# Kernel tuning notes

Hardware: AMD Instinct MI355X
Metric: run time of the kernel (lower is better)

Reference implementation:

```python
import jax, jax.numpy as jnp
import numpy as np

EPS = 1e-5
N_HEADS = 8

def layer_norm(x, g, b):
    mu = x.mean(-1, keepdims=True)
    var = ((x - mu) ** 2).mean(-1, keepdims=True)
    return (x - mu) * jax.lax.rsqrt(var + EPS) * g + b

def rotate_half(x):
    d = x.shape[-1] // 2
    return jnp.concatenate([-x[..., d:], x[..., :d]], axis=-1)

def setup_inputs() -> dict:
    key = jax.random.key(0)
    ks = jax.random.split(key, 6)
    b, n, m, h, dh = 4, 512, 8192, N_HEADS, 16
    dim = h * dh
    s = dim ** -0.5
    return {
        "x": jax.random.normal(ks[0], (b, n, dim), jnp.float32),
        "mem_kv": jax.random.normal(ks[1], (b, h, m, 2 * dh), jnp.float32),
        "w_q": jax.random.normal(ks[2], (dim, dim), jnp.float32) * s,
        "w_kv": jax.random.normal(ks[3], (2 * dim, dim), jnp.float32) * s,
        "w_out": jax.random.normal(ks[4], (dim, dim), jnp.float32) * s,
        "b_out": jnp.zeros((dim,), jnp.float32),
        "g1": jnp.ones((dim,), jnp.float32),
        "b1": jnp.zeros((dim,), jnp.float32),
        "g2": jnp.ones((dim,), jnp.float32),
        "b2": jnp.zeros((dim,), jnp.float32),
    }

def reference(x, mem_kv, w_q, w_kv, w_out, b_out, g1, b1, g2, b2):
    b, n, dim = x.shape
    h = N_HEADS
    dh = dim // h
    # pre-norm + projections
    x_ = layer_norm(x, g1, b1)
    q = (x_ @ w_q.T).reshape(b, n, h, dh).transpose(0, 2, 1, 3)          # [b,h,n,dh]
    kv = (x_ @ w_kv.T).reshape(b, n, h, 2 * dh).transpose(0, 2, 1, 3)    # [b,h,n,2dh]
    mem_kv = jnp.concatenate([mem_kv, kv], axis=2)                        # growing cache
    k, v = jnp.split(mem_kv, 2, axis=-1)                                  # [b,h,j,dh] each
    q = q * dh ** -0.5
    # rotary embeddings (SinusoidalEmbeddings over k length, q uses trailing n positions)
    j = k.shape[2]
    inv_freq = 1.0 / (10000.0 ** (jnp.arange(0, dh, 2, dtype=jnp.float32) / dh))
    fr = jnp.arange(j, dtype=jnp.float32)[:, None] * inv_freq[None, :]
    freqs = jnp.concatenate([fr, fr], axis=-1)                            # [j, dh]
    cos, sin = jnp.cos(freqs), jnp.sin(freqs)
    q = q * cos[-n:] + rotate_half(q) * sin[-n:]
    k = k * cos + rotate_half(k) * sin
    # full attention of new chunk over cache (forward_simple, inference)
    sim = jnp.einsum('bhie,bhje->bhij', q, k)
    attn = jax.nn.softmax(sim, axis=-1)
    hv = jnp.einsum('bhij,bhje->bhie', attn, v)
    hv = hv.transpose(0, 2, 1, 3).reshape(b, n, dim) + x                  # residual
    out = layer_norm(hv, g2, b2) @ w_out.T + b_out + hv                   # out proj + residual
    return out, mem_kv
```

## Files before the change

kernel.cpp:

```cpp
#include <hip/hip_runtime.h>

#define B 4
#define N 512
#define M 8192
#define H 8
#define DH 16
#define DIM 128
#define J (M + N)
#define LN10000_DIV8 1.1512925465f
#define LOG2E 1.44269504f

typedef _Float16 f16;
typedef _Float16 half4 __attribute__((ext_vector_type(4)));
typedef _Float16 half8 __attribute__((ext_vector_type(8)));
typedef __fp16 fp16x2 __attribute__((ext_vector_type(2)));
typedef float f32x4 __attribute__((ext_vector_type(4)));

#if __has_builtin(__builtin_amdgcn_exp2f)
#define EXP2(x) __builtin_amdgcn_exp2f(x)
#else
#define EXP2(x) exp2f(x)
#endif

union PK { fp16x2 v; unsigned int u; };

__device__ __forceinline__ half8 pack8(float a, float b, float c, float d,
                                       float e, float f, float g, float h) {
#if __has_builtin(__builtin_amdgcn_cvt_pkrtz)
    union { unsigned int u[4]; half8 h8; } r;
    PK p0, p1, p2, p3;
    p0.v = __builtin_amdgcn_cvt_pkrtz(a, b);
    p1.v = __builtin_amdgcn_cvt_pkrtz(c, d);
    p2.v = __builtin_amdgcn_cvt_pkrtz(e, f);
    p3.v = __builtin_amdgcn_cvt_pkrtz(g, h);
    r.u[0] = p0.u; r.u[1] = p1.u; r.u[2] = p2.u; r.u[3] = p3.u;
    return r.h8;
#else
    half8 r = { (f16)a, (f16)b, (f16)c, (f16)d, (f16)e, (f16)f, (f16)g, (f16)h };
    return r;
#endif
}

#define WS_KROT 0ull
#define WS_VT   8912896ull
#define WS_QROT 17825792ull
#define WS_HV   18350080ull
#define WS_XN   18874368ull

union K16 { f16 h[16]; uint4 u[2]; };
union V4  { f16 h[4];  uint2 u; };

__device__ __forceinline__ half8 cvt8(const float* p) {
    float4 a = *(const float4*)p, b = *(const float4*)(p + 4);
    half8 h = { (f16)a.x, (f16)a.y, (f16)a.z, (f16)a.w,
                (f16)b.x, (f16)b.y, (f16)b.z, (f16)b.w };
    return h;
}

__global__ void prep_kernel(const float4* __restrict__ src,
                            f16* __restrict__ krot, f16* __restrict__ vt,
                            const float* __restrict__ x, const float* __restrict__ g1,
                            const float* __restrict__ b1, f16* __restrict__ xn16)
{
    if (blockIdx.x < 4096) {
        __shared__ float tile[64][33];
        int bh = blockIdx.x >> 7;
        int j0 = (blockIdx.x & 127) * 64;
        int t = threadIdx.x;

        #pragma unroll
        for (int rep = 0; rep < 2; rep++) {
            int idx = t + rep * 256;
            int row = idx >> 3, c4 = idx & 7;
            float4 v = src[((size_t)bh * M + j0 + row) * 8 + c4];
            tile[row][c4 * 4 + 0] = v.x; tile[row][c4 * 4 + 1] = v.y;
            tile[row][c4 * 4 + 2] = v.z; tile[row][c4 * 4 + 3] = v.w;
        }
        __syncthreads();

        if (t < 128) {
            int row = t >> 1, rh = t & 1;
            int j = j0 + row;
            float lo4[4], hi4[4];
            #pragma unroll
            for (int i = 0; i < 4; i++) {
                int r = rh * 4 + i;
                float ang = (float)j * __expf(-(float)r * LN10000_DIV8);
                float sn, cs; __sincosf(ang, &sn, &cs);
                float lo = tile[row][r], hi = tile[row][r + 8];
                lo4[i] = lo * cs - hi * sn;
                hi4[i] = hi * cs + lo * sn;
            }
            int tilei = j >> 5, jj = j & 31;
            int col4 = (jj >> 3) * 4 + (jj & 3), frag = (jj >> 2) & 1;
            f16* base = krot + (size_t)bh * J * 16 + (size_t)tilei * 512 + col4 * 8 + frag * 4;
            V4 wl, wh;
            #pragma unroll
            for (int i = 0; i < 4; i++) { wl.h[i] = (f16)lo4[i]; wh.h[i] = (f16)hi4[i]; }
            *(uint2*)(base + rh * 128)       = wl.u;
            *(uint2*)(base + (2 + rh) * 128) = wh.u;
        }
        {
            int dh = t >> 4, c0 = (t & 15) * 4;
            V4 vv;
            #pragma unroll
            for (int i = 0; i < 4; i++) vv.h[i] = (f16)tile[c0 + i][16 + dh];
            *(uint2*)(vt + (size_t)bh * 16 * J + (size_t)dh * J + j0 + c0) = vv.u;
        }
    } else {
        int wave = threadIdx.x >> 6, lane = threadIdx.x & 63;
        int token = (blockIdx.x - 4096) * 4 + wave;
        float v0 = x[(size_t)token * DIM + lane];
        float v1 = x[(size_t)token * DIM + lane + 64];
        float s = v0 + v1;
        for (int off = 32; off; off >>= 1) s += __shfl_xor(s, off, 64);
        float mu = s * (1.0f / DIM);
        float d0 = v0 - mu, d1 = v1 - mu;
        float vs = d0 * d0 + d1 * d1;
        for (int off = 32; off; off >>= 1) vs += __shfl_xor(vs, off, 64);
        float rs = rsqrtf(vs * (1.0f / DIM) + 1e-5f);
        xn16[(size_t)token * DIM + lane]      = (f16)(d0 * rs * g1[lane]      + b1[lane]);
        xn16[(size_t)token * DIM + lane + 64] = (f16)(d1 * rs * g1[lane + 64] + b1[lane + 64]);
    }
}

__global__ void __launch_bounds__(256) proj_kernel(
    const f16* __restrict__ xn16, const float* __restrict__ wq,
    const float* __restrict__ wkv, float* __restrict__ out_mem,
    f16* __restrict__ krot, f16* __restrict__ vt, f16* __restrict__ qrot)
{
    int id = blockIdx.x * 4 + (threadIdx.x >> 6);
    int lane = threadIdx.x & 63;
    int ttile = id & 127, ctile = id >> 7;
    int token0 = ttile * 16;
    int col = lane & 15, quad = lane >> 4;

    const float* wbase = (ctile < 8) ? (wq + (size_t)(ctile * 16 + col) * DIM)
                                     : (wkv + (size_t)((ctile - 8) * 16 + col) * DIM);
    const f16* abase = xn16 + (size_t)(token0 + col) * DIM + quad * 8;

    f32x4 acc = {0.f, 0.f, 0.f, 0.f};
    #pragma unroll
    for (int kb = 0; kb < 4; kb++) {
        half8 a = *(const half8*)(abase + kb * 32);
        half8 w = cvt8(wbase + kb * 32 + quad * 8);
        acc = __builtin_amdgcn_mfma_f32_16x16x32_f16(a, w, acc, 0, 0, 0);
    }

    int e = col, r8 = e & 7;
    float f = __expf(-(float)r8 * LN10000_DIV8);
    int kt = ctile - 8;
    int head = (ctile < 8) ? ctile : (kt >> 1);
    int isV  = (ctile >= 8) ? (kt & 1) : 0;

    #pragma unroll
    for (int r = 0; r < 4; r++) {
        int tok = token0 + quad * 4 + r;
        int b = tok >> 9, i = tok & (N - 1);
        int bhh = b * H + head;
        float self = acc[r];
        float prt = __shfl_xor(self, 8, 64);

        if (ctile < 8) {
            float ang = (float)(M + i) * f;
            float sn, cs; __sincosf(ang, &sn, &cs);
            float rv = (self * cs + ((e < 8) ? -prt : prt) * sn) * (0.25f * LOG2E);
            qrot[((size_t)bhh * N + i) * 16 + e] = (f16)rv;
        } else if (!isV) {
            out_mem[((size_t)bhh * J + M + i) * 32 + e] = self;
            float ang = (float)(M + i) * f;
            float sn, cs; __sincosf(ang, &sn, &cs);
            float rv = self * cs + ((e < 8) ? -prt : prt) * sn;
            int jpos = M + i;
            int tilei = jpos >> 5, jj = jpos & 31;
            int col4 = (jj >> 3) * 4 + (jj & 3), frag = (jj >> 2) & 1;
            krot[(size_t)bhh * J * 16 + (size_t)tilei * 512 +
                 (e >> 2) * 128 + col4 * 8 + frag * 4 + (e & 3)] = (f16)rv;
        } else {
            out_mem[((size_t)bhh * J + M + i) * 32 + 16 + e] = self;
            vt[(size_t)bhh * 16 * J + (size_t)e * J + M + i] = (f16)self;
        }
    }
}

__global__ void __launch_bounds__(512, 4) attn_kernel(
    const f16* __restrict__ krot, const f16* __restrict__ vt,
    const f16* __restrict__ qrot, f16* __restrict__ hvw,
    const f32x4* __restrict__ csrc, f32x4* __restrict__ cdst)
{
    __shared__ float sacc[8][2][256];
    __shared__ float sl[8][2][16];

    if (blockIdx.x % 5 != 0) {
        int t = threadIdx.x;
        size_t copyid = (size_t)blockIdx.x - blockIdx.x / 5 - 1;
        size_t base = copyid * 1024;
        #pragma unroll
        for (int rep = 0; rep < 2; rep++) {
            size_t flat = base + rep * 512 + t;
            int bh  = (int)(flat >> 16);
            int rem = (int)(flat & 65535);
            f32x4 v = __builtin_nontemporal_load(csrc + flat);
            __builtin_nontemporal_store(v, cdst + (size_t)bh * (J * 8) + rem);
        }
        return;
    }

    int cid = blockIdx.x / 5;
    int bh = cid & 31;
    int q0 = (cid >> 5) * 32;
    int wave = threadIdx.x >> 6, lane = threadIdx.x & 63;
    int col = lane & 15, quad = lane >> 4;

    const f16* vb = vt + (size_t)bh * 16 * J + (size_t)col * J;
    half4 qfa = *(const half4*)(qrot + ((size_t)bh * N + q0 + col) * 16 + quad * 4);
    half4 qfb = *(const half4*)(qrot + ((size_t)bh * N + q0 + 16 + col) * 16 + quad * 4);

    int jstart = wave * (J / 8);
    const f16* kptr = krot + (size_t)bh * J * 16 + (size_t)jstart * 16 + lane * 8;
    const f16* vptr = vb + jstart + quad * 8;

    f32x4 acca = {0.f, 0.f, 0.f, 0.f};
    f32x4 accb = {0.f, 0.f, 0.f, 0.f};
    const f32x4 zero = {0.f, 0.f, 0.f, 0.f};
    float la = 0.f, lb = 0.f;

    #pragma unroll 2
    for (int it = 0; it < 34; ++it) {
        half8 kf8 = *(const half8*)kptr;
        half8 vf  = *(const half8*)vptr;
        kptr += 512; vptr += 32;
        half4 kf0 = __builtin_shufflevector(kf8, kf8, 0, 1, 2, 3);
        half4 kf1 = __builtin_shufflevector(kf8, kf8, 4, 5, 6, 7);
        __builtin_amdgcn_s_setprio(1);
        f32x4 s0a = __builtin_amdgcn_mfma_f32_16x16x16f16(kf0, qfa, zero, 0, 0, 0);
        f32x4 s1a = __builtin_amdgcn_mfma_f32_16x16x16f16(kf1, qfa, zero, 0, 0, 0);
        f32x4 s0b = __builtin_amdgcn_mfma_f32_16x16x16f16(kf0, qfb, zero, 0, 0, 0);
        f32x4 s1b = __builtin_amdgcn_mfma_f32_16x16x16f16(kf1, qfb, zero, 0, 0, 0);
        __builtin_amdgcn_s_setprio(0);

        float a0 = EXP2(s0a[0]), a1 = EXP2(s0a[1]), a2 = EXP2(s0a[2]), a3 = EXP2(s0a[3]);
        float a4 = EXP2(s1a[0]), a5 = EXP2(s1a[1]), a6 = EXP2(s1a[2]), a7 = EXP2(s1a[3]);
        float b0 = EXP2(s0b[0]), b1 = EXP2(s0b[1]), b2 = EXP2(s0b[2]), b3 = EXP2(s0b[3]);
        float b4 = EXP2(s1b[0]), b5 = EXP2(s1b[1]), b6 = EXP2(s1b[2]), b7 = EXP2(s1b[3]);
        la += ((a0 + a1) + (a2 + a3)) + ((a4 + a5) + (a6 + a7));
        lb += ((b0 + b1) + (b2 + b3)) + ((b4 + b5) + (b6 + b7));
        half8 pfa = pack8(a0, a1, a2, a3, a4, a5, a6, a7);
        half8 pfb = pack8(b0, b1, b2, b3, b4, b5, b6, b7);
        __builtin_amdgcn_s_setprio(1);
        acca = __builtin_amdgcn_mfma_f32_16x16x32_f16(pfa, vf, acca, 0, 0, 0);
        accb = __builtin_amdgcn_mfma_f32_16x16x32_f16(pfb, vf, accb, 0, 0, 0);
        __builtin_amdgcn_s_setprio(0);
    }

    la += __shfl_xor(la, 16, 64);
    la += __shfl_xor(la, 32, 64);
    lb += __shfl_xor(lb, 16, 64);
    lb += __shfl_xor(lb, 32, 64);
    if (quad == 0) { sl[wave][0][col] = la; sl[wave][1][col] = lb; }
    #pragma unroll
    for (int r = 0; r < 4; r++) {
        sacc[wave][0][(quad * 4 + r) * 16 + col] = acca[r];
        sacc[wave][1][(quad * 4 + r) * 16 + col] = accb[r];
    }
    __syncthreads();

    if (wave < 2) {
        int qt = wave;
        int b = bh >> 3, h = bh & 7;
        #pragma unroll
        for (int r = 0; r < 4; r++) {
            int ql = quad * 4 + r;
            float o = 0.f, lt = 0.f;
            #pragma unroll
            for (int w = 0; w < 8; w++) {
                o  += sacc[w][qt][ql * 16 + col];
                lt += sl[w][qt][ql];
            }
            hvw[((size_t)(b * N) + q0 + qt * 16 + ql) * DIM + h * DH + col] = (f16)(o / lt);
        }
    }
}

__global__ void __launch_bounds__(256) final_kernel(
    const f16* __restrict__ hvw, const float* __restrict__ x,
    const float* __restrict__ wout, const float* __restrict__ bout,
    const float* __restrict__ g2, const float* __restrict__ b2v,
    float* __restrict__ out)
{
    __shared__ f16 xn2[16][136];
    __shared__ float hres[16][132];
    int token0 = (blockIdx.x >> 1) * 16;
    int half = blockIdx.x & 1;
    int wave = threadIdx.x >> 6, lane = threadIdx.x & 63;

    #pragma unroll
    for (int tt = 0; tt < 4; tt++) {
        int tl = wave * 4 + tt;
        int token = token0 + tl;
        float h0 = (float)hvw[(size_t)token * DIM + lane]      + x[(size_t)token * DIM + lane];
        float h1 = (float)hvw[(size_t)token * DIM + lane + 64] + x[(size_t)token * DIM + lane + 64];
        float s = h0 + h1;
        for (int off = 32; off; off >>= 1) s += __shfl_xor(s, off, 64);
        float mu = s * (1.0f / DIM);
        float d0 = h0 - mu, d1 = h1 - mu;
        float vs = d0 * d0 + d1 * d1;
        for (int off = 32; off; off >>= 1) vs += __shfl_xor(vs, off, 64);
        float rs = rsqrtf(vs * (1.0f / DIM) + 1e-5f);
        xn2[tl][lane]      = (f16)(d0 * rs * g2[lane]      + b2v[lane]);
        xn2[tl][lane + 64] = (f16)(d1 * rs * g2[lane + 64] + b2v[lane + 64]);
        hres[tl][lane] = h0; hres[tl][lane + 64] = h1;
    }
    __syncthreads();

    int col = lane & 15, quad = lane >> 4;
    int ct = half * 4 + wave;
    int cg = ct * 16 + col;
    const float* wrow = wout + (size_t)cg * DIM;
    f32x4 acc = {0.f, 0.f, 0.f, 0.f};
    #pragma unroll
    for (int kb = 0; kb < 4; kb++) {
        half8 a = *(const half8*)(&xn2[col][kb * 32 + quad * 8]);
        half8 w = cvt8(wrow + kb * 32 + quad * 8);
        acc = __builtin_amdgcn_mfma_f32_16x16x32_f16(a, w, acc, 0, 0, 0);
    }
    float bo = bout[cg];
    #pragma unroll
    for (int r = 0; r < 4; r++) {
        int tl = quad * 4 + r;
        out[(size_t)(token0 + tl) * DIM + cg] = acc[r] + bo + hres[tl][cg];
    }
}

extern "C" void kernel_launch(void* const* d_in, const int* in_sizes, int n_in,
                              void* d_out, int out_size, void* d_ws, size_t ws_size,
                              hipStream_t stream)
{
    const float* x      = (const float*)d_in[0];
    const float* mem_kv = (const float*)d_in[1];
    const float* wq     = (const float*)d_in[2];
    const float* wkv    = (const float*)d_in[3];
    const float* wout   = (const float*)d_in[4];
    const float* bout   = (const float*)d_in[5];
    const float* g1     = (const float*)d_in[6];
    const float* b1     = (const float*)d_in[7];
    const float* g2     = (const float*)d_in[8];
    const float* b2     = (const float*)d_in[9];

    float* out = (float*)d_out;
    float* out_mem = out + (size_t)B * N * DIM;

    f16* krot = (f16*)((char*)d_ws + WS_KROT);
    f16* vt   = (f16*)((char*)d_ws + WS_VT);
    f16* qrot = (f16*)((char*)d_ws + WS_QROT);
    f16* hvw  = (f16*)((char*)d_ws + WS_HV);
    f16* xn16 = (f16*)((char*)d_ws + WS_XN);

    hipLaunchKernelGGL(prep_kernel, dim3(4608), dim3(256), 0, stream,
                       (const float4*)mem_kv, krot, vt, x, g1, b1, xn16);
    hipLaunchKernelGGL(proj_kernel, dim3(768), dim3(256), 0, stream,
                       xn16, wq, wkv, out_mem, krot, vt, qrot);
    hipLaunchKernelGGL(attn_kernel, dim3(2560), dim3(512), 0, stream,
                       krot, vt, qrot, hvw,
                       (const f32x4*)mem_kv, (f32x4*)out_mem);
    hipLaunchKernelGGL(final_kernel, dim3(256), dim3(256), 0, stream,
                       hvw, x, wout, bout, g2, b2, out);
}
```

Before: 157.9 us.

## Move cache copy into prep kernel, widen attention blocks, compute row sums via MFMA

The mem_kv passthrough copy moves out of the attention kernel's extra blocks and into prep_kernel, which already reads that data, so the source is read once instead of twice. The attention kernel now runs 1024-thread blocks with 16 waves, each covering half as many key positions. The softmax denominators are accumulated with extra MFMAs against a vector of ones instead of scalar adds and shuffles, and the setprio hints are dropped. Together these cut the duplicate read and the VALU reduction work, but the ones-MFMAs double the matrix instructions in the P·V stage and the reduction now spans 16 waves in LDS.

New measurement: 141.6 us. 10.3% less time.

```diff
diff --git a/kernel.cpp b/kernel.cpp
--- a/kernel.cpp
+++ b/kernel.cpp
@@ -47,7 +47,6 @@
 #define WS_HV   18350080ull
 #define WS_XN   18874368ull
 
-union K16 { f16 h[16]; uint4 u[2]; };
 union V4  { f16 h[4];  uint2 u; };
 
 __device__ __forceinline__ half8 cvt8(const float* p) {
@@ -57,7 +56,7 @@
     return h;
 }
 
-__global__ void prep_kernel(const float4* __restrict__ src,
+__global__ void prep_kernel(const float4* __restrict__ src, float4* __restrict__ dst,
                             f16* __restrict__ krot, f16* __restrict__ vt,
                             const float* __restrict__ x, const float* __restrict__ g1,
                             const float* __restrict__ b1, f16* __restrict__ xn16)
@@ -73,6 +72,7 @@
             int idx = t + rep * 256;
             int row = idx >> 3, c4 = idx & 7;
             float4 v = src[((size_t)bh * M + j0 + row) * 8 + c4];
+            dst[((size_t)bh * J + j0 + row) * 8 + c4] = v;
             tile[row][c4 * 4 + 0] = v.x; tile[row][c4 * 4 + 1] = v.y;
             tile[row][c4 * 4 + 2] = v.z; tile[row][c4 * 4 + 3] = v.w;
         }
@@ -183,32 +183,14 @@
     }
 }
 
-__global__ void __launch_bounds__(512, 4) attn_kernel(
+__global__ void __launch_bounds__(1024) attn_kernel(
     const f16* __restrict__ krot, const f16* __restrict__ vt,
-    const f16* __restrict__ qrot, f16* __restrict__ hvw,
-    const f32x4* __restrict__ csrc, f32x4* __restrict__ cdst)
-{
-    __shared__ float sacc[8][2][256];
-    __shared__ float sl[8][2][16];
-
-    if (blockIdx.x % 5 != 0) {
-        int t = threadIdx.x;
-        size_t copyid = (size_t)blockIdx.x - blockIdx.x / 5 - 1;
-        size_t base = copyid * 1024;
-        #pragma unroll
-        for (int rep = 0; rep < 2; rep++) {
-            size_t flat = base + rep * 512 + t;
-            int bh  = (int)(flat >> 16);
-            int rem = (int)(flat & 65535);
-            f32x4 v = __builtin_nontemporal_load(csrc + flat);
-            __builtin_nontemporal_store(v, cdst + (size_t)bh * (J * 8) + rem);
-        }
-        return;
-    }
-
-    int cid = blockIdx.x / 5;
-    int bh = cid & 31;
-    int q0 = (cid >> 5) * 32;
+    const f16* __restrict__ qrot, f16* __restrict__ hvw)
+{
+    __shared__ float sacc[16][2][256];
+    __shared__ float sl[16][2][16];
+    int bh = blockIdx.x & 31;
+    int q0 = (blockIdx.x >> 5) * 32;
     int wave = threadIdx.x >> 6, lane = threadIdx.x & 63;
     int col = lane & 15, quad = lane >> 4;
 
@@ -216,48 +198,49 @@
     half4 qfa = *(const half4*)(qrot + ((size_t)bh * N + q0 + col) * 16 + quad * 4);
     half4 qfb = *(const half4*)(qrot + ((size_t)bh * N + q0 + 16 + col) * 16 + quad * 4);
 
-    int jstart = wave * (J / 8);
+    int jstart = wave * (J / 16);
     const f16* kptr = krot + (size_t)bh * J * 16 + (size_t)jstart * 16 + lane * 8;
     const f16* vptr = vb + jstart + quad * 8;
 
     f32x4 acca = {0.f, 0.f, 0.f, 0.f};
     f32x4 accb = {0.f, 0.f, 0.f, 0.f};
+    f32x4 accla = {0.f, 0.f, 0.f, 0.f};
+    f32x4 acclb = {0.f, 0.f, 0.f, 0.f};
     const f32x4 zero = {0.f, 0.f, 0.f, 0.f};
-    float la = 0.f, lb = 0.f;
+    const half8 ones = { (f16)1.f, (f16)1.f, (f16)1.f, (f16)1.f,
+                         (f16)1.f, (f16)1.f, (f16)1.f, (f16)1.f };
 
     #pragma unroll 2
-    for (int it = 0; it < 34; ++it) {
+    for (int it = 0; it < 17; ++it) {
         half8 kf8 = *(const half8*)kptr;
         half8 vf  = *(const half8*)vptr;
         kptr += 512; vptr += 32;
         half4 kf0 = __builtin_shufflevector(kf8, kf8, 0, 1, 2, 3);
         half4 kf1 = __builtin_shufflevector(kf8, kf8, 4, 5, 6, 7);
-        __builtin_amdgcn_s_setprio(1);
         f32x4 s0a = __builtin_amdgcn_mfma_f32_16x16x16f16(kf0, qfa, zero, 0, 0, 0);
         f32x4 s1a = __builtin_amdgcn_mfma_f32_16x16x16f16(kf1, qfa, zero, 0, 0, 0);
         f32x4 s0b = __builtin_amdgcn_mfma_f32_16x16x16f16(kf0, qfb, zero, 0, 0, 0);
         f32x4 s1b = __builtin_amdgcn_mfma_f32_16x16x16f16(kf1, qfb, zero, 0, 0, 0);
-        __builtin_amdgcn_s_setprio(0);
 
         float a0 = EXP2(s0a[0]), a1 = EXP2(s0a[1]), a2 = EXP2(s0a[2]), a3 = EXP2(s0a[3]);
         float a4 = EXP2(s1a[0]), a5 = EXP2(s1a[1]), a6 = EXP2(s1a[2]), a7 = EXP2(s1a[3]);
         float b0 = EXP2(s0b[0]), b1 = EXP2(s0b[1]), b2 = EXP2(s0b[2]), b3 = EXP2(s0b[3]);
         float b4 = EXP2(s1b[0]), b5 = EXP2(s1b[1]), b6 = EXP2(s1b[2]), b7 = EXP2(s1b[3]);
-        la += ((a0 + a1) + (a2 + a3)) + ((a4 + a5) + (a6 + a7));
-        lb += ((b0 + b1) + (b2 + b3)) + ((b4 + b5) + (b6 + b7));
         half8 pfa = pack8(a0, a1, a2, a3, a4, a5, a6, a7);
         half8 pfb = pack8(b0, b1, b2, b3, b4, b5, b6, b7);
-        __builtin_amdgcn_s_setprio(1);
-        acca = __builtin_amdgcn_mfma_f32_16x16x32_f16(pfa, vf, acca, 0, 0, 0);
-        accb = __builtin_amdgcn_mfma_f32_16x16x32_f16(pfb, vf, accb, 0, 0, 0);
-        __builtin_amdgcn_s_setprio(0);
-    }
-
-    la += __shfl_xor(la, 16, 64);
-    la += __shfl_xor(la, 32, 64);
-    lb += __shfl_xor(lb, 16, 64);
-    lb += __shfl_xor(lb, 32, 64);
-    if (quad == 0) { sl[wave][0][col] = la; sl[wave][1][col] = lb; }
+        acca  = __builtin_amdgcn_mfma_f32_16x16x32_f16(pfa, vf,   acca,  0, 0, 0);
+        accla = __builtin_amdgcn_mfma_f32_16x16x32_f16(pfa, ones, accla, 0, 0, 0);
+        accb  = __builtin_amdgcn_mfma_f32_16x16x32_f16(pfb, vf,   accb,  0, 0, 0);
+        acclb = __builtin_amdgcn_mfma_f32_16x16x32_f16(pfb, ones, acclb, 0, 0, 0);
+    }
+
+    if (col == 0) {
+        #pragma unroll
+        for (int r = 0; r < 4; r++) {
+            sl[wave][0][quad * 4 + r] = accla[r];
+            sl[wave][1][quad * 4 + r] = acclb[r];
+        }
+    }
     #pragma unroll
     for (int r = 0; r < 4; r++) {
         sacc[wave][0][(quad * 4 + r) * 16 + col] = acca[r];
@@ -273,7 +256,7 @@
             int ql = quad * 4 + r;
             float o = 0.f, lt = 0.f;
             #pragma unroll
-            for (int w = 0; w < 8; w++) {
+            for (int w = 0; w < 16; w++) {
                 o  += sacc[w][qt][ql * 16 + col];
                 lt += sl[w][qt][ql];
             }
@@ -357,12 +340,12 @@
     f16* xn16 = (f16*)((char*)d_ws + WS_XN);
 
     hipLaunchKernelGGL(prep_kernel, dim3(4608), dim3(256), 0, stream,
-                       (const float4*)mem_kv, krot, vt, x, g1, b1, xn16);
+                       (const float4*)mem_kv, (float4*)out_mem, krot, vt,
+                       x, g1, b1, xn16);
     hipLaunchKernelGGL(proj_kernel, dim3(768), dim3(256), 0, stream,
                        xn16, wq, wkv, out_mem, krot, vt, qrot);
-    hipLaunchKernelGGL(attn_kernel, dim3(2560), dim3(512), 0, stream,
-                       krot, vt, qrot, hvw,
-                       (const f32x4*)mem_kv, (f32x4*)out_mem);
+    hipLaunchKernelGGL(attn_kernel, dim3(512), dim3(1024), 0, stream,
+                       krot, vt, qrot, hvw);
     hipLaunchKernelGGL(final_kernel, dim3(256), dim3(256), 0, stream,
                        hvw, x, wout, bout, g2, b2, out);
 }
```
